# Kernel optimization log

Measured on AMD Instinct MI355X. Metric: run time of the kernel, lower is better.

Reference implementation:

```python
import jax, jax.numpy as jnp
import numpy as np

SPARSITY = 0.8
LOCAL_WINDOW = 64


def setup_inputs() -> dict:
    key = jax.random.key(0)
    k1, k2 = jax.random.split(key)
    B, H, S = 2, 8, 2048
    attention_scores = jax.random.normal(k1, (B, H, S, S), dtype=jnp.float32)
    rand_u = jax.random.uniform(k2, (B, H, S, S), dtype=jnp.float32)
    return {"attention_scores": attention_scores, "rand_u": rand_u}


def reference(attention_scores, rand_u):
    B, H, S, _ = attention_scores.shape
    dt = attention_scores.dtype
    half = LOCAL_WINDOW // 2
    k = max(1, int(S * (1.0 - SPARSITY)))

    idx = jnp.arange(S)
    # local window mask: row i covers columns [max(0,i-half), min(S,i+half))
    local = ((idx[None, :] >= idx[:, None] - half) & (idx[None, :] < idx[:, None] + half)).astype(dt)  # (S,S)

    # global mask: topk over head-averaged importance, shared across heads
    importance = attention_scores.mean(axis=1)  # (B,S,S)
    _, top_g = jax.lax.top_k(importance, k)  # (B,S,k)
    gmask = jnp.zeros((B, S, S), dtype=dt).at[
        jnp.arange(B)[:, None, None], jnp.arange(S)[None, :, None], top_g
    ].set(1.0)

    # random sparsification mask
    random_mask = (rand_u < (1.0 - SPARSITY)).astype(dt)

    combined = ((local[None, None, :, :] + gmask[:, None, :, :] + random_mask) > 0).astype(dt)

    # sparsity enforcement: per-row topk of masked scores -> binary mask
    masked = attention_scores * combined
    _, top_f = jax.lax.top_k(masked, k)  # (B,H,S,k)
    final = jnp.zeros((B, H, S, S), dtype=dt).at[
        jnp.arange(B)[:, None, None, None],
        jnp.arange(H)[None, :, None, None],
        jnp.arange(S)[None, None, :, None],
        top_f,
    ].set(1.0)
    return final
```

## Files before the change

kernel.cpp:

```cpp
#include <hip/hip_runtime.h>
#include <cstdint>
#include <cstddef>

#define S_LEN   2048
#define N_HEADS 8
#define N_BATCH 2
#define TOPK    409
#define HALF_WIN 32
#define KEY_P0  0x80000000u
#define KEY_N0  0x7FFFFFFFu
#define HIST_STRIDE 260

__device__ __forceinline__ unsigned mbcnt64(unsigned long long m) {
  return __builtin_amdgcn_mbcnt_hi((unsigned)(m >> 32),
         __builtin_amdgcn_mbcnt_lo((unsigned)m, 0u));
}

__device__ __forceinline__ unsigned mono1(float f) {
  unsigned u = __float_as_uint(f);
  return (u & 0x80000000u) ? ~u : (u | 0x80000000u);
}

__device__ __forceinline__ void radix_range(const unsigned (&keys)[32], unsigned kk0,
                                            bool pos, unsigned* h, int l,
                                            unsigned& T_ret, unsigned& kk_ret,
                                            bool& cnt1) {
  unsigned prefix = 0, done = 0, kk = kk0;
  unsigned T = 0;
  bool resolved = false;
  cnt1 = false;
  #pragma unroll
  for (int pass = 0; pass < 4; ++pass) {
    const int shift = 24 - 8 * pass;
    *(uint4*)&h[l * 4] = make_uint4(0, 0, 0, 0);
    __threadfence_block();
    #pragma unroll
    for (int q = 0; q < 32; ++q) {
      unsigned kj = keys[q];
      bool in = pos ? (kj > KEY_P0) : (kj < KEY_N0);
      if (in && (kj & done) == prefix)
        atomicAdd(&h[(kj >> shift) & 255u], 1u);
    }
    __threadfence_block();
    uint4 hv = *(const uint4*)&h[l * 4];
    unsigned s3 = hv.w;
    unsigned s2 = hv.z + s3;
    unsigned s1 = hv.y + s2;
    unsigned s0 = hv.x + s1;
    unsigned inc = s0;
    #pragma unroll
    for (int d = 1; d < 64; d <<= 1) {
      unsigned o = __shfl_down(inc, d);
      inc += (l + d < 64) ? o : 0u;
    }
    const unsigned tail = inc - s0;
    const unsigned ge[4] = {s0 + tail, s1 + tail, s2 + tail, s3 + tail};
    const unsigned gt[4] = {s1 + tail, s2 + tail, s3 + tail, tail};
    unsigned packed = 0;
    bool found = false;
    #pragma unroll
    for (int q = 0; q < 4; ++q) {
      if (gt[q] < kk && kk <= ge[q]) {
        packed = ((unsigned)(4 * l + q) << 24) | ((ge[q] - gt[q]) << 12) | (kk - gt[q]);
        found = true;
      }
    }
    unsigned long long bal = __ballot(found);
    int srcl = __ffsll((long long)bal) - 1;
    packed = __shfl(packed, srcl);
    const unsigned cnt = (packed >> 12) & 0xFFFu;
    kk = packed & 0xFFFu;
    prefix |= (packed >> 24) << shift;
    done |= 0xFFu << shift;
    if (cnt == 1u) {
      unsigned cand = 0;
      #pragma unroll
      for (int q = 0; q < 32; ++q) {
        unsigned kj = keys[q];
        bool in = pos ? (kj > KEY_P0) : (kj < KEY_N0);
        if (in && (kj & done) == prefix) cand = kj;
      }
      #pragma unroll
      for (int d = 1; d < 64; d <<= 1) cand |= __shfl_xor(cand, d);
      T = cand;
      resolved = true;
      cnt1 = true;
      break;
    }
  }
  if (!resolved) T = prefix;
  T_ret = T;
  kk_ret = kk;
}

__device__ __forceinline__ void resolve_T(const unsigned (&keys)[32], unsigned* h,
                                          int l, unsigned& T, unsigned& kk,
                                          bool& cnt1) {
  unsigned np = 0;
  #pragma unroll
  for (int q = 0; q < 32; ++q)
    np += (unsigned)__popcll(__ballot(keys[q] > KEY_P0));
  if (TOPK <= np) {
    radix_range(keys, TOPK, true, h, l, T, kk, cnt1);
  } else {
    unsigned n0 = 0, n1 = 0;
    #pragma unroll
    for (int q = 0; q < 32; ++q) {
      unsigned kj = keys[q];
      n0 += (unsigned)__popcll(__ballot(kj == KEY_P0));
      n1 += (unsigned)__popcll(__ballot(kj == KEY_N0));
    }
    if (TOPK <= np + n0)           { T = KEY_P0; kk = TOPK - np;      cnt1 = (n0 == 1); }
    else if (TOPK <= np + n0 + n1) { T = KEY_N0; kk = TOPK - np - n0; cnt1 = (n1 == 1); }
    else radix_range(keys, TOPK - np - n0 - n1, false, h, l, T, kk, cnt1);
  }
}

__device__ __forceinline__ unsigned select_bits(const unsigned (&keys)[32],
                                                unsigned T, unsigned kk,
                                                bool cnt1, int l) {
  unsigned bits = 0;
  if (cnt1) {
    #pragma unroll
    for (int q = 0; q < 32; ++q)
      bits |= (keys[q] >= T ? 1u : 0u) << q;
    return bits;
  }
  unsigned S_tot = 0;
  #pragma unroll
  for (int s = 0; s < 8; ++s) {
    unsigned long long beq[4];
    unsigned pe[4];
    #pragma unroll
    for (int e = 0; e < 4; ++e) {
      beq[e] = __ballot(keys[4 * s + e] == T);
      pe[e] = (unsigned)__popcll(beq[e]);
    }
    const unsigned th = pe[0] + pe[1] + pe[2] + pe[3];
    if (S_tot + th <= kk) {
      #pragma unroll
      for (int e = 0; e < 4; ++e)
        bits |= (keys[4 * s + e] >= T ? 1u : 0u) << (4 * s + e);
    } else if (S_tot >= kk) {
      #pragma unroll
      for (int e = 0; e < 4; ++e)
        bits |= (keys[4 * s + e] > T ? 1u : 0u) << (4 * s + e);
    } else {
      unsigned mb[4], own[4];
      #pragma unroll
      for (int e = 0; e < 4; ++e) {
        mb[e]  = mbcnt64(beq[e]);
        own[e] = (unsigned)((beq[e] >> l) & 1ull);
      }
      const unsigned cross = S_tot + mb[0] + mb[1] + mb[2] + mb[3];
      unsigned run = 0;
      #pragma unroll
      for (int e = 0; e < 4; ++e) {
        unsigned kj = keys[4 * s + e];
        bool sel = (kj > T) || (kj == T && (cross + run) < kk);
        run += own[e];
        bits |= (sel ? 1u : 0u) << (4 * s + e);
      }
    }
    S_tot += th;
  }
  return bits;
}

__global__ __launch_bounds__(256, 4) void k_fused(const float* __restrict__ scores,
                                                  const float* __restrict__ randu,
                                                  float* __restrict__ out) {
  __shared__ __align__(16) unsigned keyrow[S_LEN];
  __shared__ __align__(16) unsigned hist[4 * HIST_STRIDE];
  const int l = threadIdx.x & 63;
  const int w = threadIdx.x >> 6;
  const int bi = blockIdx.x;
  const int b = bi >> 11;
  const int i = bi & 2047;
  const size_t gbase = (((size_t)(b * N_HEADS)) * S_LEN + i) * S_LEN;
  const float thr = (float)(1.0 - 0.8);
  unsigned* const h = hist + (size_t)w * HIST_STRIDE;
  const size_t rowA = gbase + (size_t)(2 * w) * S_LEN * S_LEN;
  const size_t rowB = rowA + (size_t)S_LEN * S_LEN;

  #pragma unroll
  for (int t = 0; t < 2; ++t) {
    const int s = 2 * w + t;
    const int c0 = 256 * s + 4 * l;
    float4 p = *(const float4*)(scores + gbase + c0);
    #pragma unroll
    for (int hh = 1; hh < N_HEADS; ++hh) {
      float4 x = *(const float4*)(scores + gbase + (size_t)hh * S_LEN * S_LEN + c0);
      p.x += x.x; p.y += x.y; p.z += x.z; p.w += x.w;
    }
    const float av[4] = {p.x, p.y, p.z, p.w};
    #pragma unroll
    for (int e = 0; e < 4; ++e)
      keyrow[(4 * s + e) * 64 + l] = mono1(av[e]);
  }
  __syncthreads();

  unsigned gql;
  {
    unsigned gk[32];
    #pragma unroll
    for (int q = 0; q < 32; ++q)
      gk[q] = keyrow[q * 64 + l];
    unsigned Tg, kkg; bool c1g;
    resolve_T(gk, h, l, Tg, kkg, c1g);
    unsigned gbits = select_bits(gk, Tg, kkg, c1g, l);
    const int lo = i - HALF_WIN;
    #pragma unroll
    for (int q = 0; q < 32; ++q) {
      const int j = 256 * (q >> 2) + 4 * l + (q & 3);
      gbits |= ((unsigned)(j - lo) < 64u ? 1u : 0u) << q;
    }
    gql = gbits;
  }

  #pragma unroll 1
  for (int t = 0; t < 2; ++t) {
    const size_t rowh = t ? rowB : rowA;
    unsigned sb[32];
    unsigned rnd = 0;
    #pragma unroll
    for (int s = 0; s < 8; ++s) {
      const int j0 = 256 * s + 4 * l;
      float4 sc = *(const float4*)(scores + rowh + j0);
      float4 ru = *(const float4*)(randu + rowh + j0);
      sb[4 * s + 0] = __float_as_uint(sc.x);
      sb[4 * s + 1] = __float_as_uint(sc.y);
      sb[4 * s + 2] = __float_as_uint(sc.z);
      sb[4 * s + 3] = __float_as_uint(sc.w);
      rnd |= (ru.x < thr ? 1u : 0u) << (4 * s + 0);
      rnd |= (ru.y < thr ? 1u : 0u) << (4 * s + 1);
      rnd |= (ru.z < thr ? 1u : 0u) << (4 * s + 2);
      rnd |= (ru.w < thr ? 1u : 0u) << (4 * s + 3);
    }
    const unsigned combined = gql | rnd;
    #pragma unroll
    for (int q = 0; q < 32; ++q) {
      const unsigned u = sb[q];
      const unsigned m = (unsigned)((int)u >> 31) | 0x80000000u;
      const bool comb = ((combined >> q) & 1u) != 0u;
      sb[q] = (comb ? u : (u & 0x80000000u)) ^ m;
    }
    unsigned T, kk; bool c1;
    resolve_T(sb, h, l, T, kk, c1);
    unsigned bits = select_bits(sb, T, kk, c1, l);
    #pragma unroll
    for (int s = 0; s < 8; ++s) {
      float v[4] __attribute__((aligned(16)));
      #pragma unroll
      for (int e = 0; e < 4; ++e)
        v[e] = ((bits >> (4 * s + e)) & 1u) ? 1.0f : 0.0f;
      *(float4*)(out + rowh + 256 * s + 4 * l) = *(const float4*)v;
    }
  }
}

extern "C" void kernel_launch(void* const* d_in, const int* in_sizes, int n_in,
                              void* d_out, int out_size, void* d_ws, size_t ws_size,
                              hipStream_t stream) {
  const float* scores = (const float*)d_in[0];
  const float* randu  = (const float*)d_in[1];
  float* out = (float*)d_out;
  (void)d_ws; (void)ws_size;
  k_fused<<<N_BATCH * S_LEN, 256, 0, stream>>>(scores, randu, out);
}
```

Baseline: 203.2 us.

## Use one wave per row block, computing global top-k once and looping heads

Shrinks each block from four waves to one wave that computes the head-averaged importance keys directly in registers. It resolves the global top-k mask once instead of redundantly in every wave, then processes all eight heads serially. This removes the LDS staging, the block barrier and duplicated global selection work, at the cost of less intra-block parallelism and longer serial work per wave.

Result: slower. 214.4 us (+5.5%).

```diff
diff --git a/kernel.cpp b/kernel.cpp
--- a/kernel.cpp
+++ b/kernel.cpp
@@ -9,7 +9,6 @@
 #define HALF_WIN 32
 #define KEY_P0  0x80000000u
 #define KEY_N0  0x7FFFFFFFu
-#define HIST_STRIDE 260
 
 __device__ __forceinline__ unsigned mbcnt64(unsigned long long m) {
   return __builtin_amdgcn_mbcnt_hi((unsigned)(m >> 32),
@@ -167,25 +166,20 @@
   return bits;
 }
 
-__global__ __launch_bounds__(256, 4) void k_fused(const float* __restrict__ scores,
-                                                  const float* __restrict__ randu,
-                                                  float* __restrict__ out) {
-  __shared__ __align__(16) unsigned keyrow[S_LEN];
-  __shared__ __align__(16) unsigned hist[4 * HIST_STRIDE];
-  const int l = threadIdx.x & 63;
-  const int w = threadIdx.x >> 6;
+__global__ __launch_bounds__(64, 4) void k_fused(const float* __restrict__ scores,
+                                                 const float* __restrict__ randu,
+                                                 float* __restrict__ out) {
+  __shared__ __align__(16) unsigned hist[256];
+  const int l = threadIdx.x;
   const int bi = blockIdx.x;
   const int b = bi >> 11;
   const int i = bi & 2047;
   const size_t gbase = (((size_t)(b * N_HEADS)) * S_LEN + i) * S_LEN;
   const float thr = (float)(1.0 - 0.8);
-  unsigned* const h = hist + (size_t)w * HIST_STRIDE;
-  const size_t rowA = gbase + (size_t)(2 * w) * S_LEN * S_LEN;
-  const size_t rowB = rowA + (size_t)S_LEN * S_LEN;
-
-  #pragma unroll
-  for (int t = 0; t < 2; ++t) {
-    const int s = 2 * w + t;
+
+  unsigned gk[32];
+  #pragma unroll
+  for (int s = 0; s < 8; ++s) {
     const int c0 = 256 * s + 4 * l;
     float4 p = *(const float4*)(scores + gbase + c0);
     #pragma unroll
@@ -193,21 +187,16 @@
       float4 x = *(const float4*)(scores + gbase + (size_t)hh * S_LEN * S_LEN + c0);
       p.x += x.x; p.y += x.y; p.z += x.z; p.w += x.w;
     }
-    const float av[4] = {p.x, p.y, p.z, p.w};
-    #pragma unroll
-    for (int e = 0; e < 4; ++e)
-      keyrow[(4 * s + e) * 64 + l] = mono1(av[e]);
-  }
-  __syncthreads();
+    gk[4 * s + 0] = mono1(p.x);
+    gk[4 * s + 1] = mono1(p.y);
+    gk[4 * s + 2] = mono1(p.z);
+    gk[4 * s + 3] = mono1(p.w);
+  }
 
   unsigned gql;
   {
-    unsigned gk[32];
-    #pragma unroll
-    for (int q = 0; q < 32; ++q)
-      gk[q] = keyrow[q * 64 + l];
     unsigned Tg, kkg; bool c1g;
-    resolve_T(gk, h, l, Tg, kkg, c1g);
+    resolve_T(gk, hist, l, Tg, kkg, c1g);
     unsigned gbits = select_bits(gk, Tg, kkg, c1g, l);
     const int lo = i - HALF_WIN;
     #pragma unroll
@@ -219,8 +208,8 @@
   }
 
   #pragma unroll 1
-  for (int t = 0; t < 2; ++t) {
-    const size_t rowh = t ? rowB : rowA;
+  for (int hh = 0; hh < N_HEADS; ++hh) {
+    const size_t rowh = gbase + (size_t)hh * S_LEN * S_LEN;
     unsigned sb[32];
     unsigned rnd = 0;
     #pragma unroll
@@ -246,7 +235,7 @@
       sb[q] = (comb ? u : (u & 0x80000000u)) ^ m;
     }
     unsigned T, kk; bool c1;
-    resolve_T(sb, h, l, T, kk, c1);
+    resolve_T(sb, hist, l, T, kk, c1);
     unsigned bits = select_bits(sb, T, kk, c1, l);
     #pragma unroll
     for (int s = 0; s < 8; ++s) {
@@ -266,5 +255,5 @@
   const float* randu  = (const float*)d_in[1];
   float* out = (float*)d_out;
   (void)d_ws; (void)ws_size;
-  k_fused<<<N_BATCH * S_LEN, 256, 0, stream>>>(scores, randu, out);
-}
+  k_fused<<<N_BATCH * S_LEN, 64, 0, stream>>>(scores, randu, out);
+}
```
